# Kernel optimization log

Measured on AMD Instinct MI355X. Metric: run time of the kernel, lower is better.

## Reference

```python
import jax, jax.numpy as jnp
import numpy as np

N = 50000    # nodes
E = 800000   # edges (avg degree 16)
IN = 256     # in_dim
HID = 256    # hidden_dim
OUT = 128    # out_dim


def setup_inputs() -> dict:
    key = jax.random.key(0)
    ks = jax.random.split(key, 9)
    features = jax.random.normal(ks[0], (N, IN), jnp.float32)
    src = jax.random.randint(ks[1], (E,), 0, N, jnp.int32)
    dst = jax.random.randint(ks[2], (E,), 0, N, jnp.int32)
    noise = jax.random.normal(ks[3], (N, OUT), jnp.float32)
    def glorot(k, shape, fan):
        return jax.random.normal(k, shape, jnp.float32) / np.float32(np.sqrt(fan))
    W1 = glorot(ks[4], (IN, HID), IN);  b1 = jnp.zeros((HID,), jnp.float32)
    W2 = glorot(ks[5], (HID, OUT), HID); b2 = jnp.zeros((OUT,), jnp.float32)
    W3 = glorot(ks[6], (HID, OUT), HID); b3 = jnp.zeros((OUT,), jnp.float32)
    fcW = glorot(ks[7], (HID, IN), IN)   # nn.Linear(in_dim, hidden_dim).weight: [HID, IN]
    return dict(features=features, noise=noise, W1=W1, b1=b1, W2=W2, b2=b2,
                W3=W3, b3=b3, fcW=fcW, src=src, dst=dst)


def _gcn(x, W, b, src, dst, out_norm, in_norm):
    """DGL GraphConv norm='both': D_out^{-1/2} A D_in^{-1/2} X W + b."""
    x = x * out_norm[:, None]          # scale src features by out-deg^{-1/2}
    x = x @ W                          # dense transform (order commutes with SpMM)
    agg = jax.ops.segment_sum(x[src], dst, num_segments=N)  # sparse aggregate
    return agg * in_norm[:, None] + b


def reference(features, noise, W1, b1, W2, b2, W3, b3, fcW, src, dst):
    ones = jnp.ones((E,), jnp.float32)
    out_deg = jax.ops.segment_sum(ones, src, num_segments=N)
    in_deg = jax.ops.segment_sum(ones, dst, num_segments=N)
    out_norm = jnp.maximum(out_deg, 1.0) ** -0.5
    in_norm = jnp.maximum(in_deg, 1.0) ** -0.5

    h = jax.nn.relu(_gcn(features, W1, b1, src, dst, out_norm, in_norm))
    mean = jax.nn.relu(_gcn(h, W2, b2, src, dst, out_norm, in_norm))
    log_std = _gcn(h, W3, b3, src, dst, out_norm, in_norm)  # identity activation
    z = mean + noise * jnp.exp(log_std)
    seq_fts = features @ fcW.T
    return z, h, seq_fts
```

## Files before the change

kernel.cpp:

```cpp
#include <hip/hip_runtime.h>
#include <hip/hip_bf16.h>
#include <stdint.h>
#include <math.h>

#define IN_DIM 256
#define HID_DIM 256
#define OUT_DIM 128

typedef __attribute__((ext_vector_type(8))) short short8;
typedef __attribute__((ext_vector_type(4))) float floatx4;

__device__ __forceinline__ float bf2f(ushort u) {
  union { uint32_t i; float f; } v; v.i = ((uint32_t)u) << 16; return v.f;
}
__device__ __forceinline__ ushort f2bf(float f) {
  union { float f; uint32_t u; } v; v.f = f;
  uint32_t u = v.u;
  uint32_t r = u + 0x7fffu + ((u >> 16) & 1u);
  return (ushort)(r >> 16);
}

__global__ void deg_kernel(const int* __restrict__ src, const int* __restrict__ dst,
                           int* __restrict__ out_deg, int* __restrict__ in_deg, int E) {
  int e = (blockIdx.x * 256 + threadIdx.x) * 2;
  if (e + 1 < E) {
    int2 s = *(const int2*)(src + e);
    int2 d = *(const int2*)(dst + e);
    atomicAdd(&out_deg[s.x], 1);
    atomicAdd(&out_deg[s.y], 1);
    atomicAdd(&in_deg[d.x], 1);
    atomicAdd(&in_deg[d.y], 1);
  } else if (e < E) {
    atomicAdd(&out_deg[src[e]], 1);
    atomicAdd(&in_deg[dst[e]], 1);
  }
}

__global__ __launch_bounds__(256, 2) void mega_kernel(
    const float* __restrict__ A32, const float* __restrict__ fcW,
    float* __restrict__ C32, ushort* __restrict__ Cbf, int M,
    const float* __restrict__ W1, const float* __restrict__ W2,
    const float* __restrict__ W3, const float* __restrict__ b2,
    const float* __restrict__ b3,
    ushort* __restrict__ W1T, ushort* __restrict__ WcT, float* __restrict__ bcat,
    const int* __restrict__ in_deg, int* __restrict__ row_ptr, int n,
    int gblocks) {
  __shared__ alignas(16) ushort A_lds[128 * 72];
  __shared__ alignas(16) ushort B_lds[256 * 72];
  int b = blockIdx.x;
  int t = threadIdx.x;

  if (b < gblocks) {
    int m0 = b * 128;
    int wave = t >> 6, lane = t & 63;
    int wm = wave * 32;
    int l15 = lane & 15, quad = lane >> 4;

    floatx4 acc[2][16];
#pragma unroll
    for (int i = 0; i < 2; ++i)
#pragma unroll
      for (int j = 0; j < 16; ++j) acc[i][j] = (floatx4)(0.f);

    for (int kc = 0; kc < 256; kc += 64) {
#pragma unroll
      for (int r = 0; r < 8; ++r) {
        int idx = t + r * 256;
        int row = idx >> 4;
        int c = (idx & 15) << 2;
        int grow = m0 + row; if (grow > M - 1) grow = M - 1;
        float4 v = *(const float4*)(A32 + (size_t)grow * 256 + kc + c);
        ushort4 o;
        o.x = f2bf(v.x); o.y = f2bf(v.y); o.z = f2bf(v.z); o.w = f2bf(v.w);
        *(ushort4*)&A_lds[row * 72 + c] = o;
        *(ushort4*)(Cbf + (size_t)grow * 256 + kc + c) = o;
      }
#pragma unroll
      for (int r = 0; r < 16; ++r) {
        int idx = t + r * 256;
        int row = idx >> 4;
        int c = (idx & 15) << 2;
        float4 v = *(const float4*)(fcW + (size_t)row * 256 + kc + c);
        ushort4 o;
        o.x = f2bf(v.x); o.y = f2bf(v.y); o.z = f2bf(v.z); o.w = f2bf(v.w);
        *(ushort4*)&B_lds[row * 72 + c] = o;
      }
      __syncthreads();
#pragma unroll
      for (int ko = 0; ko < 2; ++ko) {
        short8 a[2];
#pragma unroll
        for (int i = 0; i < 2; ++i)
          a[i] = *(const short8*)&A_lds[(wm + i * 16 + l15) * 72 + ko * 32 + quad * 8];
#pragma unroll
        for (int j = 0; j < 16; ++j) {
          short8 bb = *(const short8*)&B_lds[(j * 16 + l15) * 72 + ko * 32 + quad * 8];
#pragma unroll
          for (int i = 0; i < 2; ++i)
            acc[i][j] = __builtin_amdgcn_mfma_f32_16x16x32_bf16(a[i], bb, acc[i][j], 0, 0, 0);
        }
      }
      __syncthreads();
    }

#pragma unroll
    for (int i = 0; i < 2; ++i) {
#pragma unroll
      for (int j = 0; j < 16; ++j) {
        int col = j * 16 + l15;
#pragma unroll
        for (int r = 0; r < 4; ++r) {
          int row = m0 + wm + i * 16 + quad * 4 + r;
          if (row < M) {
            size_t o = (size_t)row * 256 + col;
            C32[o] = acc[i][j][r];
          }
        }
      }
    }
  } else if (b < gblocks + 256) {
    int k = b - gblocks;
    int nn = t;
    W1T[nn * 256 + k] = f2bf(W1[k * 256 + nn]);
    WcT[nn * 256 + k] = f2bf((nn < 128) ? W2[k * 128 + nn] : W3[k * 128 + (nn - 128)]);
    if (k == 0) bcat[nn] = (nn < 128) ? b2[nn] : b3[nn - 128];
  } else {
    int* lds = (int*)A_lds;
    const int CH = (n + 255) / 256;
    int base = t * CH;
    int lim = base + CH; if (lim > n) lim = n;
    int s = 0;
    for (int i = base; i < lim; ++i) s += in_deg[i];
    lds[t] = s;
    __syncthreads();
    for (int off = 1; off < 256; off <<= 1) {
      int add = (t >= off) ? lds[t - off] : 0;
      __syncthreads();
      lds[t] += add;
      __syncthreads();
    }
    int run = lds[t] - s;
    if (t == 0) row_ptr[0] = 0;
    for (int i = base; i < lim; ++i) {
      run += in_deg[i];
      row_ptr[i + 1] = run;
    }
  }
}

__global__ void fill_kernel(const int* __restrict__ src, const int* __restrict__ dst,
                            const int* __restrict__ row_ptr, int* __restrict__ fill_cnt,
                            const int* __restrict__ out_deg,
                            int2* __restrict__ edge_sw, int E) {
  int e = (blockIdx.x * 256 + threadIdx.x) * 2;
  if (e + 1 < E) {
    int2 s = *(const int2*)(src + e);
    int2 d = *(const int2*)(dst + e);
    int pos0 = row_ptr[d.x] + atomicAdd(&fill_cnt[d.x], 1);
    int od0 = out_deg[s.x]; if (od0 < 1) od0 = 1;
    int2 r0; r0.x = s.x; r0.y = __float_as_int(rsqrtf((float)od0));
    edge_sw[pos0] = r0;
    int pos1 = row_ptr[d.y] + atomicAdd(&fill_cnt[d.y], 1);
    int od1 = out_deg[s.y]; if (od1 < 1) od1 = 1;
    int2 r1; r1.x = s.y; r1.y = __float_as_int(rsqrtf((float)od1));
    edge_sw[pos1] = r1;
  } else if (e < E) {
    int d = dst[e]; int s = src[e];
    int pos = row_ptr[d] + atomicAdd(&fill_cnt[d], 1);
    int od = out_deg[s]; if (od < 1) od = 1;
    int2 r; r.x = s; r.y = __float_as_int(rsqrtf((float)od));
    edge_sw[pos] = r;
  }
}

__global__ __launch_bounds__(256) void agg_kernel(
    const ushort* __restrict__ x, const int* __restrict__ row_ptr,
    const int2* __restrict__ edge_sw, ushort* __restrict__ out, int N) {
  int wave = threadIdx.x >> 6, lane = threadIdx.x & 63;
  int n = blockIdx.x * 4 + wave;
  if (n >= N) return;
  int half = lane >> 5;
  int hl = lane & 31;
  int start = row_ptr[n], end = row_ptr[n + 1];
  int dg = end - start; if (dg < 1) dg = 1;
  float inn = rsqrtf((float)dg);

  float acc[8];
#pragma unroll
  for (int k = 0; k < 8; ++k) acc[k] = 0.f;

  for (int base = start; base < end; base += 16) {
    int cs[8]; float cw[8];
    if (base + 16 <= end) {
#pragma unroll
      for (int k = 0; k < 8; ++k) {
        int2 e = edge_sw[base + half + 2 * k];
        cs[k] = e.x; cw[k] = __int_as_float(e.y);
      }
    } else {
#pragma unroll
      for (int k = 0; k < 8; ++k) {
        int i = base + half + 2 * k;
        cs[k] = 0; cw[k] = 0.f;
        if (i < end) { int2 e = edge_sw[i]; cs[k] = e.x; cw[k] = __int_as_float(e.y); }
      }
    }
    uint4 v[8];
#pragma unroll
    for (int k = 0; k < 8; ++k)
      v[k] = *(const uint4*)&x[(size_t)cs[k] * 256 + hl * 8];
#pragma unroll
    for (int k = 0; k < 8; ++k) {
      const uint32_t* p = (const uint32_t*)&v[k];
      float wk = cw[k];
#pragma unroll
      for (int q = 0; q < 4; ++q) {
        acc[2 * q]     += bf2f((ushort)(p[q] & 0xffffu)) * wk;
        acc[2 * q + 1] += bf2f((ushort)(p[q] >> 16)) * wk;
      }
    }
  }

#pragma unroll
  for (int k = 0; k < 8; ++k) acc[k] += __shfl_xor(acc[k], 32, 64);

  if (half == 0) {
    uint4 o;
    uint32_t* po = (uint32_t*)&o;
#pragma unroll
    for (int q = 0; q < 4; ++q) {
      po[q] = ((uint32_t)f2bf(acc[2 * q + 1] * inn) << 16) |
              (uint32_t)f2bf(acc[2 * q] * inn);
    }
    *(uint4*)&out[(size_t)n * 256 + hl * 8] = o;
  }
}

__global__ __launch_bounds__(256, 2) void gemm_kernel(
    const ushort* __restrict__ A, const ushort* __restrict__ BT,
    const float* __restrict__ bias, const float* __restrict__ noise,
    float* __restrict__ C32, ushort* __restrict__ Cbf, int M, int mode) {
  __shared__ alignas(16) ushort A_lds[128 * 72];
  __shared__ alignas(16) ushort B_lds[256 * 72];
  int t = threadIdx.x;
  int m0 = blockIdx.x * 128;
  int wave = t >> 6, lane = t & 63;
  int wm = wave * 32;
  int l15 = lane & 15, quad = lane >> 4;

  floatx4 acc[2][16];
#pragma unroll
  for (int i = 0; i < 2; ++i)
#pragma unroll
    for (int j = 0; j < 16; ++j) acc[i][j] = (floatx4)(0.f);

  for (int kc = 0; kc < 256; kc += 64) {
#pragma unroll
    for (int r = 0; r < 4; ++r) {
      int idx = t + r * 256;
      int row = idx >> 3;
      int c = (idx & 7) << 3;
      int grow = m0 + row; if (grow > M - 1) grow = M - 1;
      *(uint4*)&A_lds[row * 72 + c] = *(const uint4*)(A + (size_t)grow * 256 + kc + c);
    }
#pragma unroll
    for (int r = 0; r < 8; ++r) {
      int idx = t + r * 256;
      int row = idx >> 3;
      int c = (idx & 7) << 3;
      *(uint4*)&B_lds[row * 72 + c] = *(const uint4*)(BT + (size_t)row * 256 + kc + c);
    }
    __syncthreads();
#pragma unroll
    for (int ko = 0; ko < 2; ++ko) {
      short8 a[2];
#pragma unroll
      for (int i = 0; i < 2; ++i)
        a[i] = *(const short8*)&A_lds[(wm + i * 16 + l15) * 72 + ko * 32 + quad * 8];
#pragma unroll
      for (int j = 0; j < 16; ++j) {
        short8 b = *(const short8*)&B_lds[(j * 16 + l15) * 72 + ko * 32 + quad * 8];
#pragma unroll
        for (int i = 0; i < 2; ++i)
          acc[i][j] = __builtin_amdgcn_mfma_f32_16x16x32_bf16(a[i], b, acc[i][j], 0, 0, 0);
      }
    }
    __syncthreads();
  }

  if (mode == 1) {
#pragma unroll
    for (int i = 0; i < 2; ++i) {
#pragma unroll
      for (int j = 0; j < 8; ++j) {
        int col = j * 16 + l15;
        float bm = bias[col];
        float bl = bias[col + 128];
#pragma unroll
        for (int r = 0; r < 4; ++r) {
          int row = m0 + wm + i * 16 + quad * 4 + r;
          if (row < M) {
            float mean = acc[i][j][r] + bm;
            float ls = acc[i][j + 8][r] + bl;
            size_t o = (size_t)row * 128 + col;
            C32[o] = fmaxf(mean, 0.f) + noise[o] * expf(ls);
          }
        }
      }
    }
  } else {
#pragma unroll
    for (int i = 0; i < 2; ++i) {
#pragma unroll
      for (int j = 0; j < 16; ++j) {
        int col = j * 16 + l15;
        float bv = bias[col];
#pragma unroll
        for (int r = 0; r < 4; ++r) {
          int row = m0 + wm + i * 16 + quad * 4 + r;
          if (row < M) {
            float v = fmaxf(acc[i][j][r] + bv, 0.f);
            size_t o = (size_t)row * 256 + col;
            C32[o] = v;
            Cbf[o] = f2bf(v);
          }
        }
      }
    }
  }
}

extern "C" void kernel_launch(void* const* d_in, const int* in_sizes, int n_in,
                              void* d_out, int out_size, void* d_ws, size_t ws_size,
                              hipStream_t stream) {
  const float* features = (const float*)d_in[0];
  const float* noise    = (const float*)d_in[1];
  const float* W1 = (const float*)d_in[2];
  const float* b1 = (const float*)d_in[3];
  const float* W2 = (const float*)d_in[4];
  const float* b2 = (const float*)d_in[5];
  const float* W3 = (const float*)d_in[6];
  const float* b3 = (const float*)d_in[7];
  const float* fcW = (const float*)d_in[8];
  const int* src = (const int*)d_in[9];
  const int* dst = (const int*)d_in[10];
  const int N = in_sizes[0] / IN_DIM;
  const int E = in_sizes[9];

  float* out = (float*)d_out;
  float* z_out = out;
  float* h_out = out + (size_t)N * OUT_DIM;
  float* s_out = h_out + (size_t)N * HID_DIM;

  char* w = (char*)d_ws;
  auto carve = [&](size_t bytes) {
    char* p = w;
    w += (bytes + 255) & ~(size_t)255;
    return p;
  };
  ushort* feat_bf = (ushort*)carve((size_t)N * 256 * 2);
  ushort* h_bf    = (ushort*)carve((size_t)N * 256 * 2);
  ushort* agg_buf = (ushort*)carve((size_t)N * 256 * 2);
  ushort* W1T  = (ushort*)carve(256 * 256 * 2);
  ushort* WcT  = (ushort*)carve(256 * 256 * 2);
  float*  bcat = (float*)carve(256 * 4);
  int* degs    = (int*)carve((size_t)3 * N * 4);
  int* out_deg = degs;
  int* in_deg  = degs + N;
  int* fill_cnt = degs + 2 * N;
  int* row_ptr  = (int*)carve((size_t)(N + 1) * 4);
  int2* edge_sw = (int2*)carve((size_t)E * 8);

  hipMemsetAsync(degs, 0, (size_t)3 * N * 4, stream);
  int eblocks = ((E + 1) / 2 + 255) / 256;
  deg_kernel<<<eblocks, 256, 0, stream>>>(src, dst, out_deg, in_deg, E);

  int gblocks = (N + 127) / 128;
  mega_kernel<<<gblocks + 257, 256, 0, stream>>>(
      features, fcW, s_out, feat_bf, N,
      W1, W2, W3, b2, b3, W1T, WcT, bcat,
      in_deg, row_ptr, N, gblocks);

  fill_kernel<<<eblocks, 256, 0, stream>>>(src, dst, row_ptr, fill_cnt, out_deg,
                                           edge_sw, E);

  agg_kernel<<<(N + 3) / 4, 256, 0, stream>>>(feat_bf, row_ptr, edge_sw, agg_buf, N);
  gemm_kernel<<<gblocks, 256, 0, stream>>>(agg_buf, W1T, b1, (const float*)nullptr,
                                           h_out, h_bf, N, 0);
  agg_kernel<<<(N + 3) / 4, 256, 0, stream>>>(h_bf, row_ptr, edge_sw, agg_buf, N);
  gemm_kernel<<<gblocks, 256, 0, stream>>>(agg_buf, WcT, bcat, noise,
                                           z_out, (ushort*)nullptr, N, 1);
}
```

Baseline: 593.5 us.

## Reorder GCN to transform-then-aggregate and fuse epilogues into aggregation

The order of each GCN layer changes from aggregate-then-GEMM to GEMM-then-aggregate. The X@W1 GEMM now runs inside the mega kernel next to the fc GEMM, and the bias, ReLU and reparameterisation epilogues move into the aggregation kernel. Weight transposition moves into the degree kernel so W1T is ready before the mega kernel, and the row_ptr scan uses vectorised int4 loads. This drops the standalone bf16 feature copy and gives GEMM epilogues with no elementwise work, in exchange for an extra bf16 rounding of XW before aggregation.

```diff
diff --git a/kernel.cpp b/kernel.cpp
--- a/kernel.cpp
+++ b/kernel.cpp
@@ -20,61 +20,114 @@
   return (ushort)(r >> 16);
 }
 
-__global__ void deg_kernel(const int* __restrict__ src, const int* __restrict__ dst,
-                           int* __restrict__ out_deg, int* __restrict__ in_deg, int E) {
-  int e = (blockIdx.x * 256 + threadIdx.x) * 2;
-  if (e + 1 < E) {
-    int2 s = *(const int2*)(src + e);
-    int2 d = *(const int2*)(dst + e);
-    atomicAdd(&out_deg[s.x], 1);
-    atomicAdd(&out_deg[s.y], 1);
-    atomicAdd(&in_deg[d.x], 1);
-    atomicAdd(&in_deg[d.y], 1);
-  } else if (e < E) {
-    atomicAdd(&out_deg[src[e]], 1);
-    atomicAdd(&in_deg[dst[e]], 1);
+__global__ void deg_prep_kernel(const int* __restrict__ src, const int* __restrict__ dst,
+                                int* __restrict__ out_deg, int* __restrict__ in_deg,
+                                int E, int eblocks,
+                                const float* __restrict__ W1, const float* __restrict__ W2,
+                                const float* __restrict__ W3, const float* __restrict__ b2,
+                                const float* __restrict__ b3,
+                                ushort* __restrict__ W1T, ushort* __restrict__ WcT,
+                                float* __restrict__ bcat) {
+  int b = blockIdx.x, t = threadIdx.x;
+  if (b < eblocks) {
+    int e = (b * 256 + t) * 2;
+    if (e + 1 < E) {
+      int2 s = *(const int2*)(src + e);
+      int2 d = *(const int2*)(dst + e);
+      atomicAdd(&out_deg[s.x], 1);
+      atomicAdd(&out_deg[s.y], 1);
+      atomicAdd(&in_deg[d.x], 1);
+      atomicAdd(&in_deg[d.y], 1);
+    } else if (e < E) {
+      atomicAdd(&out_deg[src[e]], 1);
+      atomicAdd(&in_deg[dst[e]], 1);
+    }
+  } else {
+    int k = b - eblocks;
+    int nn = t;
+    W1T[nn * 256 + k] = f2bf(W1[k * 256 + nn]);
+    WcT[nn * 256 + k] = f2bf((nn < 128) ? W2[k * 128 + nn] : W3[k * 128 + (nn - 128)]);
+    if (k == 0) bcat[nn] = (nn < 128) ? b2[nn] : b3[nn - 128];
   }
 }
 
 __global__ __launch_bounds__(256, 2) void mega_kernel(
-    const float* __restrict__ A32, const float* __restrict__ fcW,
-    float* __restrict__ C32, ushort* __restrict__ Cbf, int M,
-    const float* __restrict__ W1, const float* __restrict__ W2,
-    const float* __restrict__ W3, const float* __restrict__ b2,
-    const float* __restrict__ b3,
-    ushort* __restrict__ W1T, ushort* __restrict__ WcT, float* __restrict__ bcat,
-    const int* __restrict__ in_deg, int* __restrict__ row_ptr, int n,
-    int gblocks) {
+    const float* __restrict__ feat, const float* __restrict__ fcW,
+    const ushort* __restrict__ W1T,
+    float* __restrict__ s_out, ushort* __restrict__ xw1_bf,
+    const int* __restrict__ in_deg, int* __restrict__ row_ptr, int n, int M, int gb) {
   __shared__ alignas(16) ushort A_lds[128 * 72];
   __shared__ alignas(16) ushort B_lds[256 * 72];
   int b = blockIdx.x;
   int t = threadIdx.x;
 
-  if (b < gblocks) {
-    int m0 = b * 128;
-    int wave = t >> 6, lane = t & 63;
-    int wm = wave * 32;
-    int l15 = lane & 15, quad = lane >> 4;
-
-    floatx4 acc[2][16];
-#pragma unroll
-    for (int i = 0; i < 2; ++i)
-#pragma unroll
-      for (int j = 0; j < 16; ++j) acc[i][j] = (floatx4)(0.f);
-
-    for (int kc = 0; kc < 256; kc += 64) {
-#pragma unroll
-      for (int r = 0; r < 8; ++r) {
-        int idx = t + r * 256;
-        int row = idx >> 4;
-        int c = (idx & 15) << 2;
-        int grow = m0 + row; if (grow > M - 1) grow = M - 1;
-        float4 v = *(const float4*)(A32 + (size_t)grow * 256 + kc + c);
-        ushort4 o;
-        o.x = f2bf(v.x); o.y = f2bf(v.y); o.z = f2bf(v.z); o.w = f2bf(v.w);
-        *(ushort4*)&A_lds[row * 72 + c] = o;
-        *(ushort4*)(Cbf + (size_t)grow * 256 + kc + c) = o;
-      }
+  if (b == 0) {
+    int* lds = (int*)A_lds;
+    int CH = (n + 255) >> 8; CH = (CH + 3) & ~3;
+    int base = t * CH;
+    int s = 0;
+    if (base + CH <= n) {
+      const int4* p = (const int4*)(in_deg + base);
+      int c4 = CH >> 2;
+#pragma unroll 8
+      for (int j = 0; j < c4; ++j) { int4 q = p[j]; s += q.x + q.y + q.z + q.w; }
+    } else {
+      for (int i = base; i < n; ++i) s += in_deg[i];
+    }
+    lds[t] = s;
+    __syncthreads();
+    for (int off = 1; off < 256; off <<= 1) {
+      int add = (t >= off) ? lds[t - off] : 0;
+      __syncthreads();
+      lds[t] += add;
+      __syncthreads();
+    }
+    int run = lds[t] - s;
+    if (t == 0) row_ptr[0] = 0;
+    if (base + CH <= n) {
+      const int4* p = (const int4*)(in_deg + base);
+      int c4 = CH >> 2;
+#pragma unroll 4
+      for (int j = 0; j < c4; ++j) {
+        int4 q = p[j];
+        int i = base + j * 4;
+        run += q.x; row_ptr[i + 1] = run;
+        run += q.y; row_ptr[i + 2] = run;
+        run += q.z; row_ptr[i + 3] = run;
+        run += q.w; row_ptr[i + 4] = run;
+      }
+    } else {
+      for (int i = base; i < n; ++i) { run += in_deg[i]; row_ptr[i + 1] = run; }
+    }
+    return;
+  }
+
+  int bb = b - 1;
+  bool isSeq = bb < gb;
+  int m0 = (isSeq ? bb : bb - gb) * 128;
+  int wave = t >> 6, lane = t & 63;
+  int wm = wave * 32;
+  int l15 = lane & 15, quad = lane >> 4;
+
+  floatx4 acc[2][16];
+#pragma unroll
+  for (int i = 0; i < 2; ++i)
+#pragma unroll
+    for (int j = 0; j < 16; ++j) acc[i][j] = (floatx4)(0.f);
+
+  for (int kc = 0; kc < 256; kc += 64) {
+#pragma unroll
+    for (int r = 0; r < 8; ++r) {
+      int idx = t + r * 256;
+      int row = idx >> 4;
+      int c = (idx & 15) << 2;
+      int grow = m0 + row; if (grow > M - 1) grow = M - 1;
+      float4 v = *(const float4*)(feat + (size_t)grow * 256 + kc + c);
+      ushort4 o;
+      o.x = f2bf(v.x); o.y = f2bf(v.y); o.z = f2bf(v.z); o.w = f2bf(v.w);
+      *(ushort4*)&A_lds[row * 72 + c] = o;
+    }
+    if (isSeq) {
 #pragma unroll
       for (int r = 0; r < 16; ++r) {
         int idx = t + r * 256;
@@ -85,66 +138,57 @@
         o.x = f2bf(v.x); o.y = f2bf(v.y); o.z = f2bf(v.z); o.w = f2bf(v.w);
         *(ushort4*)&B_lds[row * 72 + c] = o;
       }
-      __syncthreads();
-#pragma unroll
-      for (int ko = 0; ko < 2; ++ko) {
-        short8 a[2];
+    } else {
+#pragma unroll
+      for (int r = 0; r < 8; ++r) {
+        int idx = t + r * 256;
+        int row = idx >> 3;
+        int c = (idx & 7) << 3;
+        *(uint4*)&B_lds[row * 72 + c] = *(const uint4*)(W1T + (size_t)row * 256 + kc + c);
+      }
+    }
+    __syncthreads();
+#pragma unroll
+    for (int ko = 0; ko < 2; ++ko) {
+      short8 a[2];
+#pragma unroll
+      for (int i = 0; i < 2; ++i)
+        a[i] = *(const short8*)&A_lds[(wm + i * 16 + l15) * 72 + ko * 32 + quad * 8];
+#pragma unroll
+      for (int j = 0; j < 16; ++j) {
+        short8 bv = *(const short8*)&B_lds[(j * 16 + l15) * 72 + ko * 32 + quad * 8];
 #pragma unroll
         for (int i = 0; i < 2; ++i)
-          a[i] = *(const short8*)&A_lds[(wm + i * 16 + l15) * 72 + ko * 32 + quad * 8];
-#pragma unroll
-        for (int j = 0; j < 16; ++j) {
-          short8 bb = *(const short8*)&B_lds[(j * 16 + l15) * 72 + ko * 32 + quad * 8];
-#pragma unroll
-          for (int i = 0; i < 2; ++i)
-            acc[i][j] = __builtin_amdgcn_mfma_f32_16x16x32_bf16(a[i], bb, acc[i][j], 0, 0, 0);
-        }
-      }
-      __syncthreads();
-    }
-
-#pragma unroll
-    for (int i = 0; i < 2; ++i) {
+          acc[i][j] = __builtin_amdgcn_mfma_f32_16x16x32_bf16(a[i], bv, acc[i][j], 0, 0, 0);
+      }
+    }
+    __syncthreads();
+  }
+
+  if (isSeq) {
+#pragma unroll
+    for (int i = 0; i < 2; ++i)
 #pragma unroll
       for (int j = 0; j < 16; ++j) {
         int col = j * 16 + l15;
 #pragma unroll
         for (int r = 0; r < 4; ++r) {
           int row = m0 + wm + i * 16 + quad * 4 + r;
-          if (row < M) {
-            size_t o = (size_t)row * 256 + col;
-            C32[o] = acc[i][j][r];
-          }
+          if (row < M) s_out[(size_t)row * 256 + col] = acc[i][j][r];
         }
       }
-    }
-  } else if (b < gblocks + 256) {
-    int k = b - gblocks;
-    int nn = t;
-    W1T[nn * 256 + k] = f2bf(W1[k * 256 + nn]);
-    WcT[nn * 256 + k] = f2bf((nn < 128) ? W2[k * 128 + nn] : W3[k * 128 + (nn - 128)]);
-    if (k == 0) bcat[nn] = (nn < 128) ? b2[nn] : b3[nn - 128];
   } else {
-    int* lds = (int*)A_lds;
-    const int CH = (n + 255) / 256;
-    int base = t * CH;
-    int lim = base + CH; if (lim > n) lim = n;
-    int s = 0;
-    for (int i = base; i < lim; ++i) s += in_deg[i];
-    lds[t] = s;
-    __syncthreads();
-    for (int off = 1; off < 256; off <<= 1) {
-      int add = (t >= off) ? lds[t - off] : 0;
-      __syncthreads();
-      lds[t] += add;
-      __syncthreads();
-    }
-    int run = lds[t] - s;
-    if (t == 0) row_ptr[0] = 0;
-    for (int i = base; i < lim; ++i) {
-      run += in_deg[i];
-      row_ptr[i + 1] = run;
-    }
+#pragma unroll
+    for (int i = 0; i < 2; ++i)
+#pragma unroll
+      for (int j = 0; j < 16; ++j) {
+        int col = j * 16 + l15;
+#pragma unroll
+        for (int r = 0; r < 4; ++r) {
+          int row = m0 + wm + i * 16 + quad * 4 + r;
+          if (row < M) xw1_bf[(size_t)row * 256 + col] = f2bf(acc[i][j][r]);
+        }
+      }
   }
 }
 
@@ -175,7 +219,9 @@
 
 __global__ __launch_bounds__(256) void agg_kernel(
     const ushort* __restrict__ x, const int* __restrict__ row_ptr,
-    const int2* __restrict__ edge_sw, ushort* __restrict__ out, int N) {
+    const int2* __restrict__ edge_sw,
+    const float* __restrict__ bias, const float* __restrict__ noise,
+    float* __restrict__ out32, ushort* __restrict__ outbf, int N, int mode) {
   int wave = threadIdx.x >> 6, lane = threadIdx.x & 63;
   int n = blockIdx.x * 4 + wave;
   if (n >= N) return;
@@ -224,22 +270,60 @@
 #pragma unroll
   for (int k = 0; k < 8; ++k) acc[k] += __shfl_xor(acc[k], 32, 64);
 
-  if (half == 0) {
-    uint4 o;
-    uint32_t* po = (uint32_t*)&o;
-#pragma unroll
-    for (int q = 0; q < 4; ++q) {
-      po[q] = ((uint32_t)f2bf(acc[2 * q + 1] * inn) << 16) |
-              (uint32_t)f2bf(acc[2 * q] * inn);
-    }
-    *(uint4*)&out[(size_t)n * 256 + hl * 8] = o;
-  }
-}
-
-__global__ __launch_bounds__(256, 2) void gemm_kernel(
+  if (mode == 0) {
+    if (half == 0) {
+      int c0 = hl * 8;
+      float4 ba = *(const float4*)(bias + c0);
+      float4 bb = *(const float4*)(bias + c0 + 4);
+      float h[8];
+      h[0] = fmaxf(acc[0] * inn + ba.x, 0.f);
+      h[1] = fmaxf(acc[1] * inn + ba.y, 0.f);
+      h[2] = fmaxf(acc[2] * inn + ba.z, 0.f);
+      h[3] = fmaxf(acc[3] * inn + ba.w, 0.f);
+      h[4] = fmaxf(acc[4] * inn + bb.x, 0.f);
+      h[5] = fmaxf(acc[5] * inn + bb.y, 0.f);
+      h[6] = fmaxf(acc[6] * inn + bb.z, 0.f);
+      h[7] = fmaxf(acc[7] * inn + bb.w, 0.f);
+      float4 o0 = make_float4(h[0], h[1], h[2], h[3]);
+      float4 o1 = make_float4(h[4], h[5], h[6], h[7]);
+      *(float4*)&out32[(size_t)n * 256 + c0] = o0;
+      *(float4*)&out32[(size_t)n * 256 + c0 + 4] = o1;
+      uint4 ob; uint32_t* po = (uint32_t*)&ob;
+#pragma unroll
+      for (int q = 0; q < 4; ++q)
+        po[q] = ((uint32_t)f2bf(h[2 * q + 1]) << 16) | (uint32_t)f2bf(h[2 * q]);
+      *(uint4*)&outbf[(size_t)n * 256 + c0] = ob;
+    }
+  } else {
+    float pacc[8];
+#pragma unroll
+    for (int k = 0; k < 8; ++k) pacc[k] = __shfl(acc[k], (lane & 15) + 16, 64);
+    if (lane < 16) {
+      int c0 = lane * 8;
+      float4 b2a = *(const float4*)(bias + c0);
+      float4 b2b = *(const float4*)(bias + c0 + 4);
+      float4 b3a = *(const float4*)(bias + 128 + c0);
+      float4 b3b = *(const float4*)(bias + 128 + c0 + 4);
+      float4 nza = *(const float4*)(noise + (size_t)n * 128 + c0);
+      float4 nzb = *(const float4*)(noise + (size_t)n * 128 + c0 + 4);
+      float z[8];
+      z[0] = fmaxf(acc[0] * inn + b2a.x, 0.f) + nza.x * expf(pacc[0] * inn + b3a.x);
+      z[1] = fmaxf(acc[1] * inn + b2a.y, 0.f) + nza.y * expf(pacc[1] * inn + b3a.y);
+      z[2] = fmaxf(acc[2] * inn + b2a.z, 0.f) + nza.z * expf(pacc[2] * inn + b3a.z);
+      z[3] = fmaxf(acc[3] * inn + b2a.w, 0.f) + nza.w * expf(pacc[3] * inn + b3a.w);
+      z[4] = fmaxf(acc[4] * inn + b2b.x, 0.f) + nzb.x * expf(pacc[4] * inn + b3b.x);
+      z[5] = fmaxf(acc[5] * inn + b2b.y, 0.f) + nzb.y * expf(pacc[5] * inn + b3b.y);
+      z[6] = fmaxf(acc[6] * inn + b2b.z, 0.f) + nzb.z * expf(pacc[6] * inn + b3b.z);
+      z[7] = fmaxf(acc[7] * inn + b2b.w, 0.f) + nzb.w * expf(pacc[7] * inn + b3b.w);
+      *(float4*)&out32[(size_t)n * 128 + c0] = make_float4(z[0], z[1], z[2], z[3]);
+      *(float4*)&out32[(size_t)n * 128 + c0 + 4] = make_float4(z[4], z[5], z[6], z[7]);
+    }
+  }
+}
+
+__global__ __launch_bounds__(256, 2) void gemm_bf_kernel(
     const ushort* __restrict__ A, const ushort* __restrict__ BT,
-    const float* __restrict__ bias, const float* __restrict__ noise,
-    float* __restrict__ C32, ushort* __restrict__ Cbf, int M, int mode) {
+    ushort* __restrict__ Cbf, int M) {
   __shared__ alignas(16) ushort A_lds[128 * 72];
   __shared__ alignas(16) ushort B_lds[256 * 72];
   int t = threadIdx.x;
@@ -279,55 +363,26 @@
         a[i] = *(const short8*)&A_lds[(wm + i * 16 + l15) * 72 + ko * 32 + quad * 8];
 #pragma unroll
       for (int j = 0; j < 16; ++j) {
-        short8 b = *(const short8*)&B_lds[(j * 16 + l15) * 72 + ko * 32 + quad * 8];
+        short8 bv = *(const short8*)&B_lds[(j * 16 + l15) * 72 + ko * 32 + quad * 8];
 #pragma unroll
         for (int i = 0; i < 2; ++i)
-          acc[i][j] = __builtin_amdgcn_mfma_f32_16x16x32_bf16(a[i], b, acc[i][j], 0, 0, 0);
+          acc[i][j] = __builtin_amdgcn_mfma_f32_16x16x32_bf16(a[i], bv, acc[i][j], 0, 0, 0);
       }
     }
     __syncthreads();
   }
 
-  if (mode == 1) {
-#pragma unroll
-    for (int i = 0; i < 2; ++i) {
-#pragma unroll
-      for (int j = 0; j < 8; ++j) {
-        int col = j * 16 + l15;
-        float bm = bias[col];
-        float bl = bias[col + 128];
-#pragma unroll
-        for (int r = 0; r < 4; ++r) {
-          int row = m0 + wm + i * 16 + quad * 4 + r;
-          if (row < M) {
-            float mean = acc[i][j][r] + bm;
-            float ls = acc[i][j + 8][r] + bl;
-            size_t o = (size_t)row * 128 + col;
-            C32[o] = fmaxf(mean, 0.f) + noise[o] * expf(ls);
-          }
-        }
-      }
-    }
-  } else {
-#pragma unroll
-    for (int i = 0; i < 2; ++i) {
-#pragma unroll
-      for (int j = 0; j < 16; ++j) {
-        int col = j * 16 + l15;
-        float bv = bias[col];
-#pragma unroll
-        for (int r = 0; r < 4; ++r) {
-          int row = m0 + wm + i * 16 + quad * 4 + r;
-          if (row < M) {
-            float v = fmaxf(acc[i][j][r] + bv, 0.f);
-            size_t o = (size_t)row * 256 + col;
-            C32[o] = v;
-            Cbf[o] = f2bf(v);
-          }
-        }
-      }
-    }
-  }
+#pragma unroll
+  for (int i = 0; i < 2; ++i)
+#pragma unroll
+    for (int j = 0; j < 16; ++j) {
+      int col = j * 16 + l15;
+#pragma unroll
+      for (int r = 0; r < 4; ++r) {
+        int row = m0 + wm + i * 16 + quad * 4 + r;
+        if (row < M) Cbf[(size_t)row * 256 + col] = f2bf(acc[i][j][r]);
+      }
+    }
 }
 
 extern "C" void kernel_launch(void* const* d_in, const int* in_sizes, int n_in,
@@ -358,9 +413,9 @@
     w += (bytes + 255) & ~(size_t)255;
     return p;
   };
-  ushort* feat_bf = (ushort*)carve((size_t)N * 256 * 2);
-  ushort* h_bf    = (ushort*)carve((size_t)N * 256 * 2);
-  ushort* agg_buf = (ushort*)carve((size_t)N * 256 * 2);
+  ushort* xw1_bf = (ushort*)carve((size_t)N * 256 * 2);
+  ushort* h_bf   = (ushort*)carve((size_t)N * 256 * 2);
+  ushort* hwc_bf = (ushort*)carve((size_t)N * 256 * 2);
   ushort* W1T  = (ushort*)carve(256 * 256 * 2);
   ushort* WcT  = (ushort*)carve(256 * 256 * 2);
   float*  bcat = (float*)carve(256 * 4);
@@ -373,21 +428,17 @@
 
   hipMemsetAsync(degs, 0, (size_t)3 * N * 4, stream);
   int eblocks = ((E + 1) / 2 + 255) / 256;
-  deg_kernel<<<eblocks, 256, 0, stream>>>(src, dst, out_deg, in_deg, E);
-
-  int gblocks = (N + 127) / 128;
-  mega_kernel<<<gblocks + 257, 256, 0, stream>>>(
-      features, fcW, s_out, feat_bf, N,
-      W1, W2, W3, b2, b3, W1T, WcT, bcat,
-      in_deg, row_ptr, N, gblocks);
-
+  int gb = (N + 127) / 128;
+
+  deg_prep_kernel<<<eblocks + 256, 256, 0, stream>>>(src, dst, out_deg, in_deg, E, eblocks,
+                                                     W1, W2, W3, b2, b3, W1T, WcT, bcat);
+  mega_kernel<<<2 * gb + 1, 256, 0, stream>>>(features, fcW, W1T, s_out, xw1_bf,
+                                              in_deg, row_ptr, N, N, gb);
   fill_kernel<<<eblocks, 256, 0, stream>>>(src, dst, row_ptr, fill_cnt, out_deg,
                                            edge_sw, E);
-
-  agg_kernel<<<(N + 3) / 4, 256, 0, stream>>>(feat_bf, row_ptr, edge_sw, agg_buf, N);
-  gemm_kernel<<<gblocks, 256, 0, stream>>>(agg_buf, W1T, b1, (const float*)nullptr,
-                                           h_out, h_bf, N, 0);
-  agg_kernel<<<(N + 3) / 4, 256, 0, stream>>>(h_bf, row_ptr, edge_sw, agg_buf, N);
-  gemm_kernel<<<gblocks, 256, 0, stream>>>(agg_buf, WcT, bcat, noise,
-                                           z_out, (ushort*)nullptr, N, 1);
-}
+  agg_kernel<<<(N + 3) / 4, 256, 0, stream>>>(xw1_bf, row_ptr, edge_sw, b1,
+                                              (const float*)nullptr, h_out, h_bf, N, 0);
+  gemm_bf_kernel<<<gb, 256, 0, stream>>>(h_bf, WcT, hwc_bf, N);
+  agg_kernel<<<(N + 3) / 4, 256, 0, stream>>>(hwc_bf, row_ptr, edge_sw, bcat,
+                                              noise, z_out, (ushort*)nullptr, N, 1);
+}
```

Measured after the change: 508.7 us. -14.3%, faster.
